# Kernel tuning notes

Measured on AMD Instinct MI355X. Metric: run time of the kernel, lower is better.

Reference implementation:

```python
import jax, jax.numpy as jnp
import numpy as np
from jax import lax

FEAT = 384        # features
FFN = 768         # ffn_features (chunk=True -> halves of 384)
ZDIM = FFN // 2   # 384
HID = 192         # AE hidden
B, N = 4, 128
LN_EPS = 1e-5


def gelu(x):
    return jax.nn.gelu(x, approximate=False)  # torch nn.GELU default = exact erf


def setup_inputs() -> dict:
    key = jax.random.key(0)
    ks = jax.random.split(key, 12)

    def lin(k, fan_in, shape):
        bound = 1.0 / np.sqrt(fan_in)
        return jax.random.uniform(k, shape, jnp.float32, -bound, bound)

    return {
        "x": jax.random.normal(ks[0], (B, N, FEAT), jnp.float32),
        "U_w": lin(ks[1], FEAT, (FEAT, FFN)),
        "U_b": lin(ks[2], FEAT, (FFN,)),
        "ln_w": jnp.ones((ZDIM,), jnp.float32),
        "ln_b": jnp.zeros((ZDIM,), jnp.float32),
        "enc_w": lin(ks[3], ZDIM, (ZDIM, HID)),
        "enc_b": lin(ks[4], ZDIM, (HID,)),
        "dec_w": lin(ks[5], HID, (HID, ZDIM)),
        "dec_b": lin(ks[6], HID, (ZDIM,)),
        "V_w": lin(ks[7], ZDIM, (ZDIM, FEAT)),
        "V_b": lin(ks[8], ZDIM, (FEAT,)),
    }


def _ae(z, enc_w, enc_b, dec_w, dec_b):
    h = gelu(z @ enc_w + enc_b)
    return h @ dec_w + dec_b


def reference(x, U_w, U_b, ln_w, ln_b, enc_w, enc_b, dec_w, dec_b, V_w, V_b):
    h = gelu(x @ U_w + U_b)                    # (B,N,FFN)
    xh, z = jnp.split(h, 2, axis=-1)           # chunk=True: (B,N,ZDIM) each
    z = lax.stop_gradient(z)                   # z.detach()
    mu = jnp.mean(z, axis=-1, keepdims=True)
    var = jnp.var(z, axis=-1, keepdims=True)
    z = (z - mu) / jnp.sqrt(var + LN_EPS) * ln_w + ln_b

    n = z.shape[1]
    eye = jnp.eye(n, dtype=z.dtype)
    # z_mask[b,i,j,:] = z[b,j,:] if i==j else 0   (mask_type='zeros')
    z_mask = eye[None, :, :, None] * z[:, None, :, :]   # (B,N,N,ZDIM)
    preds = _ae(z_mask, enc_w, enc_b, dec_w, dec_b)      # (B,N,N,ZDIM)
    dist = jnp.einsum('bijf,bjf->bij', preds, z)         # (B,N,N)
    attn = lax.stop_gradient(jax.nn.softmax(dist, axis=-1))
    out = jnp.einsum('bij,bjf->bif', attn, xh)           # (B,N,ZDIM)
    return out @ V_w + V_b                               # (B,N,FEAT)
```

## Files before the change

### kernel.cpp

```cpp
#include <hip/hip_runtime.h>
#include <hip/hip_bf16.h>
#include <math.h>

#define FEAT 384
#define FFN  768
#define ZDIM 384
#define HID  192
#define BB   4
#define NN   128
#define BN   (BB*NN)

__device__ __forceinline__ float gelu_exact(float x) {
    return 0.5f * x * (1.0f + erff(x * 0.70710678118654752440f));
}

__device__ __forceinline__ float bflo(unsigned u) { return __uint_as_float(u << 16); }
__device__ __forceinline__ float bfhi(unsigned u) { return __uint_as_float(u & 0xFFFF0000u); }

template<bool F32>
__device__ __forceinline__ float ldg(const void* p, int i) {
    if constexpr (F32) return ((const float*)p)[i];
    return __uint_as_float(((unsigned)((const unsigned short*)p)[i]) << 16);
}

__device__ __forceinline__ unsigned pack2(float a, float b) {
    __hip_bfloat16 ba = __float2bfloat16(a), bb = __float2bfloat16(b);
    unsigned short ua, ub;
    __builtin_memcpy(&ua, &ba, 2);
    __builtin_memcpy(&ub, &bb, 2);
    return (unsigned)ua | ((unsigned)ub << 16);
}

template<bool F32>
__device__ __forceinline__ void st8(void* p, size_t off, const float v[8]) {
    if constexpr (F32) {
        *(float4*)((float*)p + off)     = make_float4(v[0], v[1], v[2], v[3]);
        *(float4*)((float*)p + off + 4) = make_float4(v[4], v[5], v[6], v[7]);
    } else {
        uint4 u;
        u.x = pack2(v[0], v[1]); u.y = pack2(v[2], v[3]);
        u.z = pack2(v[4], v[5]); u.w = pack2(v[6], v[7]);
        *(uint4*)((unsigned short*)p + off) = u;
    }
}

template<bool F32> struct V8;
template<> struct V8<true> {
    float4 a, b;
    __device__ __forceinline__ void load(const void* p, size_t off) {
        a = *(const float4*)((const float*)p + off);
        b = *(const float4*)((const float*)p + off + 4);
    }
    __device__ __forceinline__ float g(int i) const {
        return (i < 4) ? (&a.x)[i] : (&b.x)[i - 4];
    }
};
template<> struct V8<false> {
    uint4 u;
    __device__ __forceinline__ void load(const void* p, size_t off) {
        u = *(const uint4*)((const unsigned short*)p + off);
    }
    __device__ __forceinline__ float g(int i) const {
        const unsigned w = (&u.x)[i >> 1];
        return (i & 1) ? bfhi(w) : bflo(w);
    }
};
template<bool F32> struct V4;
template<> struct V4<true> {
    float4 a;
    __device__ __forceinline__ void load(const void* p, size_t off) {
        a = *(const float4*)((const float*)p + off);
    }
    __device__ __forceinline__ float g(int i) const { return (&a.x)[i]; }
};
template<> struct V4<false> {
    uint2 u;
    __device__ __forceinline__ void load(const void* p, size_t off) {
        u = *(const uint2*)((const unsigned short*)p + off);
    }
    __device__ __forceinline__ float g(int i) const {
        const unsigned w = (&u.x)[i >> 1];
        return (i & 1) ? bfhi(w) : bflo(w);
    }
};

__device__ __forceinline__ bool is_f32(const void* ln_w) {
    return ((const unsigned short*)ln_w)[0] == 0;
}

__device__ __forceinline__ float block_sum(float v, float* sm) {
    for (int o = 32; o > 0; o >>= 1) v += __shfl_down(v, o, 64);
    const int lane = threadIdx.x & 63, w = threadIdx.x >> 6;
    __syncthreads();
    if (lane == 0) sm[w] = v;
    __syncthreads();
    return sm[0] + sm[1] + sm[2] + sm[3] + sm[4] + sm[5];
}
__device__ __forceinline__ float2 block_sum2(float vx, float vy, float* sm) {
    for (int o = 32; o > 0; o >>= 1) {
        vx += __shfl_down(vx, o, 64);
        vy += __shfl_down(vy, o, 64);
    }
    const int lane = threadIdx.x & 63, w = threadIdx.x >> 6;
    __syncthreads();
    if (lane == 0) { sm[w] = vx; sm[w + 6] = vy; }
    __syncthreads();
    return make_float2(sm[0] + sm[1] + sm[2] + sm[3] + sm[4] + sm[5],
                       sm[6] + sm[7] + sm[8] + sm[9] + sm[10] + sm[11]);
}
__device__ __forceinline__ float block_max(float v, float* sm) {
    for (int o = 32; o > 0; o >>= 1) v = fmaxf(v, __shfl_down(v, o, 64));
    const int lane = threadIdx.x & 63, w = threadIdx.x >> 6;
    __syncthreads();
    if (lane == 0) sm[w] = v;
    __syncthreads();
    return fmaxf(fmaxf(fmaxf(sm[0], sm[1]), fmaxf(sm[2], sm[3])), fmaxf(sm[4], sm[5]));
}

template<bool F32>
__device__ void rows_body(
    const void* __restrict__ x, const void* __restrict__ U_w,
    const void* __restrict__ U_b, const void* __restrict__ ln_w,
    const void* __restrict__ ln_b, const void* __restrict__ enc_w,
    const void* __restrict__ enc_b, const void* __restrict__ dec_w,
    const void* __restrict__ dec_b,
    float* __restrict__ xh, float* __restrict__ d0, float* __restrict__ diag)
{
    const int g = blockIdx.x;
    const int r0 = 2 * g, r1 = r0 + 1;
    const int t = threadIdx.x;
    __shared__ float xs[2][FEAT];
    __shared__ float zs[2][ZDIM];
    __shared__ float hid[2][HID];
    __shared__ float gh[HID];
    __shared__ float part[4608];
    __shared__ float sm[12];

    xs[0][t] = ldg<F32>(x, r0 * FEAT + t);
    xs[1][t] = ldg<F32>(x, r1 * FEAT + t);
    if (t < HID) gh[t] = gelu_exact(ldg<F32>(enc_b, t));
    __syncthreads();

    const int cgU = t % 96, khU = t / 96;
    const int cU = 8 * cgU;
    float acc0[8] = {0,0,0,0,0,0,0,0}, acc1[8] = {0,0,0,0,0,0,0,0};
    {
        const int kb = 96 * khU;
        V8<F32> wa[8], wb[8];
        #pragma unroll
        for (int j = 0; j < 8; j++) wa[j].load(U_w, (size_t)(kb + j) * FFN + cU);
        for (int k0 = kb; k0 < kb + 96; k0 += 16) {
            #pragma unroll
            for (int j = 0; j < 8; j++) wb[j].load(U_w, (size_t)(k0 + 8 + j) * FFN + cU);
            #pragma unroll
            for (int j = 0; j < 8; j++) {
                const float x0 = xs[0][k0 + j], x1 = xs[1][k0 + j];
                #pragma unroll
                for (int i = 0; i < 8; i++) {
                    const float w = wa[j].g(i);
                    acc0[i] = fmaf(x0, w, acc0[i]);
                    acc1[i] = fmaf(x1, w, acc1[i]);
                }
            }
            if (k0 + 16 < kb + 96) {
                #pragma unroll
                for (int j = 0; j < 8; j++) wa[j].load(U_w, (size_t)(k0 + 16 + j) * FFN + cU);
            }
            #pragma unroll
            for (int j = 0; j < 8; j++) {
                const float x0 = xs[0][k0 + 8 + j], x1 = xs[1][k0 + 8 + j];
                #pragma unroll
                for (int i = 0; i < 8; i++) {
                    const float w = wb[j].g(i);
                    acc0[i] = fmaf(x0, w, acc0[i]);
                    acc1[i] = fmaf(x1, w, acc1[i]);
                }
            }
        }
    }
    if (khU > 0) {
        float* p0 = &part[(size_t)(khU - 1) * 1536 + cU];
        #pragma unroll
        for (int i = 0; i < 8; i++) { p0[i] = acc0[i]; p0[768 + i] = acc1[i]; }
    }
    __syncthreads();

    float h0[8], h1[8];
    float s1a = 0.f, s1b = 0.f, s2a = 0.f, s2b = 0.f;
    if (khU == 0) {
        #pragma unroll
        for (int i = 0; i < 8; i++) {
            const int c = cU + i;
            const float ub = ldg<F32>(U_b, c);
            float v0 = acc0[i] + part[c] + part[1536 + c] + part[3072 + c] + ub;
            float v1 = acc1[i] + part[768 + c] + part[1536 + 768 + c] + part[3072 + 768 + c] + ub;
            v0 = gelu_exact(v0); v1 = gelu_exact(v1);
            h0[i] = v0; h1[i] = v1;
            if (cgU >= 48) { s1a += v0; s2a += v0 * v0; s1b += v1; s2b += v1 * v1; }
        }
        if (cgU < 48) {
            *(float4*)(xh + (size_t)r0 * ZDIM + cU)     = make_float4(h0[0], h0[1], h0[2], h0[3]);
            *(float4*)(xh + (size_t)r0 * ZDIM + cU + 4) = make_float4(h0[4], h0[5], h0[6], h0[7]);
            *(float4*)(xh + (size_t)r1 * ZDIM + cU)     = make_float4(h1[0], h1[1], h1[2], h1[3]);
            *(float4*)(xh + (size_t)r1 * ZDIM + cU + 4) = make_float4(h1[4], h1[5], h1[6], h1[7]);
        }
    }
    const float2 S1 = block_sum2(s1a, s1b, sm);
    const float2 S2 = block_sum2(s2a, s2b, sm);
    const float mu0 = S1.x * (1.0f / ZDIM), mu1 = S1.y * (1.0f / ZDIM);
    const float rs0 = rsqrtf(S2.x * (1.0f / ZDIM) - mu0 * mu0 + 1e-5f);
    const float rs1 = rsqrtf(S2.y * (1.0f / ZDIM) - mu1 * mu1 + 1e-5f);
    if (khU == 0 && cgU >= 48) {
        #pragma unroll
        for (int i = 0; i < 8; i++) {
            const int zc = cU - ZDIM + i;
            const float w = ldg<F32>(ln_w, zc), bb = ldg<F32>(ln_b, zc);
            zs[0][zc] = (h0[i] - mu0) * rs0 * w + bb;
            zs[1][zc] = (h1[i] - mu1) * rs1 * w + bb;
        }
    }
    __syncthreads();

    {
        const int cg = t % 48, kh = t / 48;
        const int cE = 4 * cg, kb = 48 * kh;
        float e0a[4] = {0,0,0,0}, e1a[4] = {0,0,0,0};
        V4<F32> ea[8], eb[8];
        #pragma unroll
        for (int j = 0; j < 8; j++) ea[j].load(enc_w, (size_t)(kb + j) * HID + cE);
        for (int k0 = kb; k0 < kb + 48; k0 += 16) {
            #pragma unroll
            for (int j = 0; j < 8; j++) eb[j].load(enc_w, (size_t)(k0 + 8 + j) * HID + cE);
            #pragma unroll
            for (int j = 0; j < 8; j++) {
                const float z0 = zs[0][k0 + j], z1 = zs[1][k0 + j];
                #pragma unroll
                for (int i = 0; i < 4; i++) {
                    const float w = ea[j].g(i);
                    e0a[i] = fmaf(z0, w, e0a[i]);
                    e1a[i] = fmaf(z1, w, e1a[i]);
                }
            }
            if (k0 + 16 < kb + 48) {
                #pragma unroll
                for (int j = 0; j < 8; j++) ea[j].load(enc_w, (size_t)(k0 + 16 + j) * HID + cE);
            }
            #pragma unroll
            for (int j = 0; j < 8; j++) {
                const float z0 = zs[0][k0 + 8 + j], z1 = zs[1][k0 + 8 + j];
                #pragma unroll
                for (int i = 0; i < 4; i++) {
                    const float w = eb[j].g(i);
                    e0a[i] = fmaf(z0, w, e0a[i]);
                    e1a[i] = fmaf(z1, w, e1a[i]);
                }
            }
        }
        if (kh > 0) {
            float* p = &part[(size_t)(kh - 1) * 384 + cE];
            #pragma unroll
            for (int i = 0; i < 4; i++) { p[i] = e0a[i]; p[192 + i] = e1a[i]; }
        }
        __syncthreads();
        if (kh == 0) {
            #pragma unroll
            for (int i = 0; i < 4; i++) {
                const int c = cE + i;
                float v0 = e0a[i], v1 = e1a[i];
                #pragma unroll
                for (int kk = 0; kk < 7; kk++) {
                    v0 += part[kk * 384 + c];
                    v1 += part[kk * 384 + 192 + c];
                }
                const float ebv = ldg<F32>(enc_b, c);
                hid[0][c] = gelu_exact(v0 + ebv);
                hid[1][c] = gelu_exact(v1 + ebv);
            }
        }
        __syncthreads();
    }

    {
        const int cg = t % 96, kh = t / 96;
        const int cD = 4 * cg, kb = 48 * kh;
        float a0[4] = {0,0,0,0}, a1[4] = {0,0,0,0}, a2[4] = {0,0,0,0};
        V4<F32> da[8], db_[8];
        #pragma unroll
        for (int j = 0; j < 8; j++) da[j].load(dec_w, (size_t)(kb + j) * ZDIM + cD);
        for (int k0 = kb; k0 < kb + 48; k0 += 16) {
            #pragma unroll
            for (int j = 0; j < 8; j++) db_[j].load(dec_w, (size_t)(k0 + 8 + j) * ZDIM + cD);
            #pragma unroll
            for (int j = 0; j < 8; j++) {
                const float v0 = hid[0][k0 + j], v1 = hid[1][k0 + j], gv = gh[k0 + j];
                #pragma unroll
                for (int i = 0; i < 4; i++) {
                    const float w = da[j].g(i);
                    a0[i] = fmaf(v0, w, a0[i]);
                    a1[i] = fmaf(v1, w, a1[i]);
                    a2[i] = fmaf(gv, w, a2[i]);
                }
            }
            if (k0 + 16 < kb + 48) {
                #pragma unroll
                for (int j = 0; j < 8; j++) da[j].load(dec_w, (size_t)(k0 + 16 + j) * ZDIM + cD);
            }
            #pragma unroll
            for (int j = 0; j < 8; j++) {
                const float v0 = hid[0][k0 + 8 + j], v1 = hid[1][k0 + 8 + j], gv = gh[k0 + 8 + j];
                #pragma unroll
                for (int i = 0; i < 4; i++) {
                    const float w = db_[j].g(i);
                    a0[i] = fmaf(v0, w, a0[i]);
                    a1[i] = fmaf(v1, w, a1[i]);
                    a2[i] = fmaf(gv, w, a2[i]);
                }
            }
        }
        if (kh > 0) {
            float* p = &part[(size_t)(kh - 1) * 1152 + cD];
            #pragma unroll
            for (int i = 0; i < 4; i++) { p[i] = a0[i]; p[384 + i] = a1[i]; p[768 + i] = a2[i]; }
        }
        __syncthreads();
        float pd0 = 0.f, pd1 = 0.f, pe0 = 0.f, pe1 = 0.f;
        if (kh == 0) {
            #pragma unroll
            for (int i = 0; i < 4; i++) {
                const int c = cD + i;
                const float dbv = ldg<F32>(dec_b, c);
                const float v0 = a0[i] + part[c] + part[1152 + c] + part[2304 + c] + dbv;
                const float v1 = a1[i] + part[384 + c] + part[1152 + 384 + c] + part[2304 + 384 + c] + dbv;
                const float v2 = a2[i] + part[768 + c] + part[1152 + 768 + c] + part[2304 + 768 + c] + dbv;
                const float z0 = zs[0][c], z1 = zs[1][c];
                pd0 = fmaf(v0, z0, pd0);
                pd1 = fmaf(v1, z1, pd1);
                pe0 = fmaf(v2, z0, pe0);
                pe1 = fmaf(v2, z1, pe1);
            }
        }
        const float2 DG = block_sum2(pd0, pd1, sm);
        const float2 DD = block_sum2(pe0, pe1, sm);
        if (t == 0) {
            diag[r0] = DG.x; diag[r1] = DG.y;
            d0[r0] = DD.x;   d0[r1] = DD.y;
        }
    }
}

__global__ __launch_bounds__(384) void k_rows(
    const void* x, const void* U_w, const void* U_b,
    const void* ln_w, const void* ln_b,
    const void* enc_w, const void* enc_b,
    const void* dec_w, const void* dec_b,
    float* xh, float* d0, float* diag)
{
    if (is_f32(ln_w))
        rows_body<true >(x, U_w, U_b, ln_w, ln_b, enc_w, enc_b, dec_w, dec_b, xh, d0, diag);
    else
        rows_body<false>(x, U_w, U_b, ln_w, ln_b, enc_w, enc_b, dec_w, dec_b, xh, d0, diag);
}

template<bool F32>
__device__ void out_body(
    const float* __restrict__ d0, const float* __restrict__ diag,
    const float* __restrict__ xh,
    const void* __restrict__ V_w, const void* __restrict__ V_b,
    void* __restrict__ out)
{
    const int g = blockIdx.x;
    const int r0 = 2 * g, r1 = r0 + 1;
    const int b = r0 >> 7;
    const int t = threadIdx.x;
    __shared__ float e0s[NN];
    __shared__ float as[2][ZDIM];
    __shared__ float pv[5376];
    __shared__ float sm[12];

    float d0v = -INFINITY, dgv = -INFINITY;
    if (t < NN) { d0v = d0[b * NN + t]; dgv = diag[b * NN + t]; }
    const float m = block_max(fmaxf(d0v, dgv), sm);
    float e0v = 0.f;
    if (t < NN) { e0v = expf(d0v - m); e0s[t] = e0v; }
    const float S = block_sum(e0v, sm);

    const float e00 = expf(d0[r0] - m), e01 = expf(d0[r1] - m);
    const float ed0 = expf(diag[r0] - m), ed1 = expf(diag[r1] - m);
    const float inv0 = 1.0f / (S - e00 + ed0);
    const float inv1 = 1.0f / (S - e01 + ed1);

    float acc = 0.f;
    {
        const float* xp = xh + (size_t)b * NN * ZDIM + t;
        float wa[16], wb[16];
        #pragma unroll
        for (int j = 0; j < 16; j++) wa[j] = xp[(size_t)j * ZDIM];
        for (int j0 = 0; j0 < NN; j0 += 32) {
            #pragma unroll
            for (int j = 0; j < 16; j++) wb[j] = xp[(size_t)(j0 + 16 + j) * ZDIM];
            #pragma unroll
            for (int j = 0; j < 16; j++) acc = fmaf(e0s[j0 + j], wa[j], acc);
            if (j0 + 32 < NN) {
                #pragma unroll
                for (int j = 0; j < 16; j++) wa[j] = xp[(size_t)(j0 + 32 + j) * ZDIM];
            }
            #pragma unroll
            for (int j = 0; j < 16; j++) acc = fmaf(e0s[j0 + 16 + j], wb[j], acc);
        }
    }
    as[0][t] = (acc + (ed0 - e00) * xh[(size_t)r0 * ZDIM + t]) * inv0;
    as[1][t] = (acc + (ed1 - e01) * xh[(size_t)r1 * ZDIM + t]) * inv1;
    __syncthreads();

    const int cg = t % 48, kh = t / 48;
    const int cV = 8 * cg, kb = 48 * kh;
    float a0[8] = {0,0,0,0,0,0,0,0}, a1[8] = {0,0,0,0,0,0,0,0};
    {
        V8<F32> va[8], vb[8];
        #pragma unroll
        for (int j = 0; j < 8; j++) va[j].load(V_w, (size_t)(kb + j) * FEAT + cV);
        for (int f0 = kb; f0 < kb + 48; f0 += 16) {
            #pragma unroll
            for (int j = 0; j < 8; j++) vb[j].load(V_w, (size_t)(f0 + 8 + j) * FEAT + cV);
            #pragma unroll
            for (int j = 0; j < 8; j++) {
                const float s0 = as[0][f0 + j], s1 = as[1][f0 + j];
                #pragma unroll
                for (int i = 0; i < 8; i++) {
                    const float w = va[j].g(i);
                    a0[i] = fmaf(s0, w, a0[i]);
                    a1[i] = fmaf(s1, w, a1[i]);
                }
            }
            if (f0 + 16 < kb + 48) {
                #pragma unroll
                for (int j = 0; j < 8; j++) va[j].load(V_w, (size_t)(f0 + 16 + j) * FEAT + cV);
            }
            #pragma unroll
            for (int j = 0; j < 8; j++) {
                const float s0 = as[0][f0 + 8 + j], s1 = as[1][f0 + 8 + j];
                #pragma unroll
                for (int i = 0; i < 8; i++) {
                    const float w = vb[j].g(i);
                    a0[i] = fmaf(s0, w, a0[i]);
                    a1[i] = fmaf(s1, w, a1[i]);
                }
            }
        }
    }
    if (kh > 0) {
        float* p = &pv[(size_t)(kh - 1) * 768 + cV];
        #pragma unroll
        for (int i = 0; i < 8; i++) { p[i] = a0[i]; p[384 + i] = a1[i]; }
    }
    __syncthreads();
    if (kh == 0) {
        float o0[8], o1[8];
        #pragma unroll
        for (int i = 0; i < 8; i++) {
            const int c = cV + i;
            const float vb_ = ldg<F32>(V_b, c);
            float u0 = a0[i] + vb_, u1 = a1[i] + vb_;
            #pragma unroll
            for (int kk = 0; kk < 7; kk++) {
                u0 += pv[kk * 768 + c];
                u1 += pv[kk * 768 + 384 + c];
            }
            o0[i] = u0; o1[i] = u1;
        }
        st8<F32>(out, (size_t)r0 * FEAT + cV, o0);
        st8<F32>(out, (size_t)r1 * FEAT + cV, o1);
    }
}

__global__ __launch_bounds__(384) void k_out(
    const void* ln_w,
    const float* d0, const float* diag, const float* xh,
    const void* V_w, const void* V_b, void* out)
{
    if (is_f32(ln_w))
        out_body<true >(d0, diag, xh, V_w, V_b, out);
    else
        out_body<false>(d0, diag, xh, V_w, V_b, out);
}

extern "C" void kernel_launch(void* const* d_in, const int* in_sizes, int n_in,
                              void* d_out, int out_size, void* d_ws, size_t ws_size,
                              hipStream_t stream) {
    const void* x     = d_in[0];
    const void* U_w   = d_in[1];
    const void* U_b   = d_in[2];
    const void* ln_w  = d_in[3];
    const void* ln_b  = d_in[4];
    const void* enc_w = d_in[5];
    const void* enc_b = d_in[6];
    const void* dec_w = d_in[7];
    const void* dec_b = d_in[8];
    const void* V_w   = d_in[9];
    const void* V_b   = d_in[10];

    float* ws   = (float*)d_ws;
    float* xh   = ws;
    float* d0   = xh + (size_t)BN * ZDIM;
    float* diag = d0 + BN;

    k_rows<<<BN / 2, 384, 0, stream>>>(x, U_w, U_b, ln_w, ln_b, enc_w, enc_b,
                                       dec_w, dec_b, xh, d0, diag);
    k_out<<<BN / 2, 384, 0, stream>>>(ln_w, d0, diag, xh, V_w, V_b, d_out);
}
```

Before: 111.7 us.

## Split per-row work across more blocks: one row per block, halves of FFN

Changes k_rows from two rows per block to one row per block, further split into two blocks that each compute one half of the U projection. The xh half writes its output and exits, and the z half runs LayerNorm, the autoencoder and the dot products. k_out likewise moves to one row per block. The aim is to raise parallelism from 256 blocks to 1024 and 512 so more CUs stay busy, at the cost of losing weight reuse across two rows and reading the weights more often.

Result: slower. 157.0 us (+40.5%).

```diff
diff --git a/kernel.cpp b/kernel.cpp
--- a/kernel.cpp
+++ b/kernel.cpp
@@ -126,225 +126,194 @@
     const void* __restrict__ dec_b,
     float* __restrict__ xh, float* __restrict__ d0, float* __restrict__ diag)
 {
-    const int g = blockIdx.x;
-    const int r0 = 2 * g, r1 = r0 + 1;
+    const int r = blockIdx.x >> 1;
+    const int h = blockIdx.x & 1;
     const int t = threadIdx.x;
-    __shared__ float xs[2][FEAT];
-    __shared__ float zs[2][ZDIM];
-    __shared__ float hid[2][HID];
+    __shared__ float xs[FEAT];
+    __shared__ float zs[ZDIM];
+    __shared__ float hid[HID];
     __shared__ float gh[HID];
-    __shared__ float part[4608];
+    __shared__ float part[7 * 384];
     __shared__ float sm[12];
 
-    xs[0][t] = ldg<F32>(x, r0 * FEAT + t);
-    xs[1][t] = ldg<F32>(x, r1 * FEAT + t);
-    if (t < HID) gh[t] = gelu_exact(ldg<F32>(enc_b, t));
-    __syncthreads();
-
-    const int cgU = t % 96, khU = t / 96;
-    const int cU = 8 * cgU;
-    float acc0[8] = {0,0,0,0,0,0,0,0}, acc1[8] = {0,0,0,0,0,0,0,0};
+    xs[t] = ldg<F32>(x, r * FEAT + t);
+    if (h && t < HID) gh[t] = gelu_exact(ldg<F32>(enc_b, t));
+    __syncthreads();
+
+    const int cg = t % 48, kh = t / 48;
+    const int cLoc = 8 * cg;
+    const int cGlob = 384 * h + cLoc;
+    const int kb = 48 * kh;
+    float acc[8] = {0,0,0,0,0,0,0,0};
     {
-        const int kb = 96 * khU;
         V8<F32> wa[8], wb[8];
         #pragma unroll
-        for (int j = 0; j < 8; j++) wa[j].load(U_w, (size_t)(kb + j) * FFN + cU);
-        for (int k0 = kb; k0 < kb + 96; k0 += 16) {
-            #pragma unroll
-            for (int j = 0; j < 8; j++) wb[j].load(U_w, (size_t)(k0 + 8 + j) * FFN + cU);
-            #pragma unroll
-            for (int j = 0; j < 8; j++) {
-                const float x0 = xs[0][k0 + j], x1 = xs[1][k0 + j];
-                #pragma unroll
-                for (int i = 0; i < 8; i++) {
-                    const float w = wa[j].g(i);
-                    acc0[i] = fmaf(x0, w, acc0[i]);
-                    acc1[i] = fmaf(x1, w, acc1[i]);
-                }
-            }
-            if (k0 + 16 < kb + 96) {
-                #pragma unroll
-                for (int j = 0; j < 8; j++) wa[j].load(U_w, (size_t)(k0 + 16 + j) * FFN + cU);
-            }
-            #pragma unroll
-            for (int j = 0; j < 8; j++) {
-                const float x0 = xs[0][k0 + 8 + j], x1 = xs[1][k0 + 8 + j];
-                #pragma unroll
-                for (int i = 0; i < 8; i++) {
-                    const float w = wb[j].g(i);
-                    acc0[i] = fmaf(x0, w, acc0[i]);
-                    acc1[i] = fmaf(x1, w, acc1[i]);
-                }
-            }
-        }
-    }
-    if (khU > 0) {
-        float* p0 = &part[(size_t)(khU - 1) * 1536 + cU];
-        #pragma unroll
-        for (int i = 0; i < 8; i++) { p0[i] = acc0[i]; p0[768 + i] = acc1[i]; }
-    }
-    __syncthreads();
-
-    float h0[8], h1[8];
-    float s1a = 0.f, s1b = 0.f, s2a = 0.f, s2b = 0.f;
-    if (khU == 0) {
+        for (int j = 0; j < 8; j++) wa[j].load(U_w, (size_t)(kb + j) * FFN + cGlob);
+        for (int k0 = kb; k0 < kb + 48; k0 += 16) {
+            #pragma unroll
+            for (int j = 0; j < 8; j++) wb[j].load(U_w, (size_t)(k0 + 8 + j) * FFN + cGlob);
+            #pragma unroll
+            for (int j = 0; j < 8; j++) {
+                const float xv = xs[k0 + j];
+                #pragma unroll
+                for (int i = 0; i < 8; i++) acc[i] = fmaf(xv, wa[j].g(i), acc[i]);
+            }
+            if (k0 + 16 < kb + 48) {
+                #pragma unroll
+                for (int j = 0; j < 8; j++) wa[j].load(U_w, (size_t)(k0 + 16 + j) * FFN + cGlob);
+            }
+            #pragma unroll
+            for (int j = 0; j < 8; j++) {
+                const float xv = xs[k0 + 8 + j];
+                #pragma unroll
+                for (int i = 0; i < 8; i++) acc[i] = fmaf(xv, wb[j].g(i), acc[i]);
+            }
+        }
+    }
+    if (kh > 0) {
+        float* p = &part[(kh - 1) * 384 + cLoc];
+        #pragma unroll
+        for (int i = 0; i < 8; i++) p[i] = acc[i];
+    }
+    __syncthreads();
+
+    float hv[8];
+    float s1 = 0.f, s2 = 0.f;
+    if (kh == 0) {
         #pragma unroll
         for (int i = 0; i < 8; i++) {
-            const int c = cU + i;
-            const float ub = ldg<F32>(U_b, c);
-            float v0 = acc0[i] + part[c] + part[1536 + c] + part[3072 + c] + ub;
-            float v1 = acc1[i] + part[768 + c] + part[1536 + 768 + c] + part[3072 + 768 + c] + ub;
-            v0 = gelu_exact(v0); v1 = gelu_exact(v1);
-            h0[i] = v0; h1[i] = v1;
-            if (cgU >= 48) { s1a += v0; s2a += v0 * v0; s1b += v1; s2b += v1 * v1; }
-        }
-        if (cgU < 48) {
-            *(float4*)(xh + (size_t)r0 * ZDIM + cU)     = make_float4(h0[0], h0[1], h0[2], h0[3]);
-            *(float4*)(xh + (size_t)r0 * ZDIM + cU + 4) = make_float4(h0[4], h0[5], h0[6], h0[7]);
-            *(float4*)(xh + (size_t)r1 * ZDIM + cU)     = make_float4(h1[0], h1[1], h1[2], h1[3]);
-            *(float4*)(xh + (size_t)r1 * ZDIM + cU + 4) = make_float4(h1[4], h1[5], h1[6], h1[7]);
-        }
-    }
-    const float2 S1 = block_sum2(s1a, s1b, sm);
-    const float2 S2 = block_sum2(s2a, s2b, sm);
-    const float mu0 = S1.x * (1.0f / ZDIM), mu1 = S1.y * (1.0f / ZDIM);
-    const float rs0 = rsqrtf(S2.x * (1.0f / ZDIM) - mu0 * mu0 + 1e-5f);
-    const float rs1 = rsqrtf(S2.y * (1.0f / ZDIM) - mu1 * mu1 + 1e-5f);
-    if (khU == 0 && cgU >= 48) {
+            float v = acc[i] + ldg<F32>(U_b, cGlob + i);
+            #pragma unroll
+            for (int kk = 0; kk < 7; kk++) v += part[kk * 384 + cLoc + i];
+            v = gelu_exact(v);
+            hv[i] = v;
+            s1 += v; s2 += v * v;
+        }
+        if (h == 0) {
+            *(float4*)(xh + (size_t)r * ZDIM + cLoc)     = make_float4(hv[0], hv[1], hv[2], hv[3]);
+            *(float4*)(xh + (size_t)r * ZDIM + cLoc + 4) = make_float4(hv[4], hv[5], hv[6], hv[7]);
+        }
+    }
+    if (h == 0) return;
+
+    const float2 S = block_sum2(s1, s2, sm);
+    const float mu = S.x * (1.0f / ZDIM);
+    const float rs = rsqrtf(S.y * (1.0f / ZDIM) - mu * mu + 1e-5f);
+    if (kh == 0) {
         #pragma unroll
         for (int i = 0; i < 8; i++) {
-            const int zc = cU - ZDIM + i;
-            const float w = ldg<F32>(ln_w, zc), bb = ldg<F32>(ln_b, zc);
-            zs[0][zc] = (h0[i] - mu0) * rs0 * w + bb;
-            zs[1][zc] = (h1[i] - mu1) * rs1 * w + bb;
+            const int zc = cLoc + i;
+            zs[zc] = (hv[i] - mu) * rs * ldg<F32>(ln_w, zc) + ldg<F32>(ln_b, zc);
         }
     }
     __syncthreads();
 
     {
-        const int cg = t % 48, kh = t / 48;
-        const int cE = 4 * cg, kb = 48 * kh;
-        float e0a[4] = {0,0,0,0}, e1a[4] = {0,0,0,0};
-        V4<F32> ea[8], eb[8];
-        #pragma unroll
-        for (int j = 0; j < 8; j++) ea[j].load(enc_w, (size_t)(kb + j) * HID + cE);
-        for (int k0 = kb; k0 < kb + 48; k0 += 16) {
-            #pragma unroll
-            for (int j = 0; j < 8; j++) eb[j].load(enc_w, (size_t)(k0 + 8 + j) * HID + cE);
-            #pragma unroll
-            for (int j = 0; j < 8; j++) {
-                const float z0 = zs[0][k0 + j], z1 = zs[1][k0 + j];
-                #pragma unroll
-                for (int i = 0; i < 4; i++) {
-                    const float w = ea[j].g(i);
-                    e0a[i] = fmaf(z0, w, e0a[i]);
-                    e1a[i] = fmaf(z1, w, e1a[i]);
-                }
-            }
-            if (k0 + 16 < kb + 48) {
-                #pragma unroll
-                for (int j = 0; j < 8; j++) ea[j].load(enc_w, (size_t)(k0 + 16 + j) * HID + cE);
-            }
-            #pragma unroll
-            for (int j = 0; j < 8; j++) {
-                const float z0 = zs[0][k0 + 8 + j], z1 = zs[1][k0 + 8 + j];
-                #pragma unroll
-                for (int i = 0; i < 4; i++) {
-                    const float w = eb[j].g(i);
-                    e0a[i] = fmaf(z0, w, e0a[i]);
-                    e1a[i] = fmaf(z1, w, e1a[i]);
-                }
-            }
-        }
-        if (kh > 0) {
-            float* p = &part[(size_t)(kh - 1) * 384 + cE];
-            #pragma unroll
-            for (int i = 0; i < 4; i++) { p[i] = e0a[i]; p[192 + i] = e1a[i]; }
+        const int cgE = t % 48, khE = t / 48;
+        const int cE = 4 * cgE, kbE = 48 * khE;
+        float ea[4] = {0,0,0,0};
+        V4<F32> va[8], vb[8];
+        #pragma unroll
+        for (int j = 0; j < 8; j++) va[j].load(enc_w, (size_t)(kbE + j) * HID + cE);
+        for (int k0 = kbE; k0 < kbE + 48; k0 += 16) {
+            #pragma unroll
+            for (int j = 0; j < 8; j++) vb[j].load(enc_w, (size_t)(k0 + 8 + j) * HID + cE);
+            #pragma unroll
+            for (int j = 0; j < 8; j++) {
+                const float zv = zs[k0 + j];
+                #pragma unroll
+                for (int i = 0; i < 4; i++) ea[i] = fmaf(zv, va[j].g(i), ea[i]);
+            }
+            if (k0 + 16 < kbE + 48) {
+                #pragma unroll
+                for (int j = 0; j < 8; j++) va[j].load(enc_w, (size_t)(k0 + 16 + j) * HID + cE);
+            }
+            #pragma unroll
+            for (int j = 0; j < 8; j++) {
+                const float zv = zs[k0 + 8 + j];
+                #pragma unroll
+                for (int i = 0; i < 4; i++) ea[i] = fmaf(zv, vb[j].g(i), ea[i]);
+            }
+        }
+        if (khE > 0) {
+            float* p = &part[(khE - 1) * 192 + cE];
+            #pragma unroll
+            for (int i = 0; i < 4; i++) p[i] = ea[i];
         }
         __syncthreads();
-        if (kh == 0) {
+        if (khE == 0) {
             #pragma unroll
             for (int i = 0; i < 4; i++) {
                 const int c = cE + i;
-                float v0 = e0a[i], v1 = e1a[i];
-                #pragma unroll
-                for (int kk = 0; kk < 7; kk++) {
-                    v0 += part[kk * 384 + c];
-                    v1 += part[kk * 384 + 192 + c];
+                float v = ea[i] + ldg<F32>(enc_b, c);
+                #pragma unroll
+                for (int kk = 0; kk < 7; kk++) v += part[kk * 192 + c];
+                hid[c] = gelu_exact(v);
+            }
+        }
+        __syncthreads();
+    }
+
+    {
+        const int cgD = t % 96, khD = t / 96;
+        const int cD = 4 * cgD, kbD = 48 * khD;
+        float aa[4] = {0,0,0,0}, ac[4] = {0,0,0,0};
+        V4<F32> va[8], vb[8];
+        #pragma unroll
+        for (int j = 0; j < 8; j++) va[j].load(dec_w, (size_t)(kbD + j) * ZDIM + cD);
+        for (int k0 = kbD; k0 < kbD + 48; k0 += 16) {
+            #pragma unroll
+            for (int j = 0; j < 8; j++) vb[j].load(dec_w, (size_t)(k0 + 8 + j) * ZDIM + cD);
+            #pragma unroll
+            for (int j = 0; j < 8; j++) {
+                const float hvv = hid[k0 + j], gv = gh[k0 + j];
+                #pragma unroll
+                for (int i = 0; i < 4; i++) {
+                    const float w = va[j].g(i);
+                    aa[i] = fmaf(hvv, w, aa[i]);
+                    ac[i] = fmaf(gv, w, ac[i]);
                 }
-                const float ebv = ldg<F32>(enc_b, c);
-                hid[0][c] = gelu_exact(v0 + ebv);
-                hid[1][c] = gelu_exact(v1 + ebv);
-            }
+            }
+            if (k0 + 16 < kbD + 48) {
+                #pragma unroll
+                for (int j = 0; j < 8; j++) va[j].load(dec_w, (size_t)(k0 + 16 + j) * ZDIM + cD);
+            }
+            #pragma unroll
+            for (int j = 0; j < 8; j++) {
+                const float hvv = hid[k0 + 8 + j], gv = gh[k0 + 8 + j];
+                #pragma unroll
+                for (int i = 0; i < 4; i++) {
+                    const float w = vb[j].g(i);
+                    aa[i] = fmaf(hvv, w, aa[i]);
+                    ac[i] = fmaf(gv, w, ac[i]);
+                }
+            }
+        }
+        if (khD > 0) {
+            float* p = &part[(khD - 1) * 768 + cD];
+            #pragma unroll
+            for (int i = 0; i < 4; i++) { p[i] = aa[i]; p[384 + i] = ac[i]; }
         }
         __syncthreads();
-    }
-
-    {
-        const int cg = t % 96, kh = t / 96;
-        const int cD = 4 * cg, kb = 48 * kh;
-        float a0[4] = {0,0,0,0}, a1[4] = {0,0,0,0}, a2[4] = {0,0,0,0};
-        V4<F32> da[8], db_[8];
-        #pragma unroll
-        for (int j = 0; j < 8; j++) da[j].load(dec_w, (size_t)(kb + j) * ZDIM + cD);
-        for (int k0 = kb; k0 < kb + 48; k0 += 16) {
-            #pragma unroll
-            for (int j = 0; j < 8; j++) db_[j].load(dec_w, (size_t)(k0 + 8 + j) * ZDIM + cD);
-            #pragma unroll
-            for (int j = 0; j < 8; j++) {
-                const float v0 = hid[0][k0 + j], v1 = hid[1][k0 + j], gv = gh[k0 + j];
-                #pragma unroll
-                for (int i = 0; i < 4; i++) {
-                    const float w = da[j].g(i);
-                    a0[i] = fmaf(v0, w, a0[i]);
-                    a1[i] = fmaf(v1, w, a1[i]);
-                    a2[i] = fmaf(gv, w, a2[i]);
-                }
-            }
-            if (k0 + 16 < kb + 48) {
-                #pragma unroll
-                for (int j = 0; j < 8; j++) da[j].load(dec_w, (size_t)(k0 + 16 + j) * ZDIM + cD);
-            }
-            #pragma unroll
-            for (int j = 0; j < 8; j++) {
-                const float v0 = hid[0][k0 + 8 + j], v1 = hid[1][k0 + 8 + j], gv = gh[k0 + 8 + j];
-                #pragma unroll
-                for (int i = 0; i < 4; i++) {
-                    const float w = db_[j].g(i);
-                    a0[i] = fmaf(v0, w, a0[i]);
-                    a1[i] = fmaf(v1, w, a1[i]);
-                    a2[i] = fmaf(gv, w, a2[i]);
-                }
-            }
-        }
-        if (kh > 0) {
-            float* p = &part[(size_t)(kh - 1) * 1152 + cD];
-            #pragma unroll
-            for (int i = 0; i < 4; i++) { p[i] = a0[i]; p[384 + i] = a1[i]; p[768 + i] = a2[i]; }
-        }
-        __syncthreads();
-        float pd0 = 0.f, pd1 = 0.f, pe0 = 0.f, pe1 = 0.f;
-        if (kh == 0) {
+        float pd = 0.f, pe = 0.f;
+        if (khD == 0) {
             #pragma unroll
             for (int i = 0; i < 4; i++) {
                 const int c = cD + i;
                 const float dbv = ldg<F32>(dec_b, c);
-                const float v0 = a0[i] + part[c] + part[1152 + c] + part[2304 + c] + dbv;
-                const float v1 = a1[i] + part[384 + c] + part[1152 + 384 + c] + part[2304 + 384 + c] + dbv;
-                const float v2 = a2[i] + part[768 + c] + part[1152 + 768 + c] + part[2304 + 768 + c] + dbv;
-                const float z0 = zs[0][c], z1 = zs[1][c];
-                pd0 = fmaf(v0, z0, pd0);
-                pd1 = fmaf(v1, z1, pd1);
-                pe0 = fmaf(v2, z0, pe0);
-                pe1 = fmaf(v2, z1, pe1);
-            }
-        }
-        const float2 DG = block_sum2(pd0, pd1, sm);
-        const float2 DD = block_sum2(pe0, pe1, sm);
-        if (t == 0) {
-            diag[r0] = DG.x; diag[r1] = DG.y;
-            d0[r0] = DD.x;   d0[r1] = DD.y;
-        }
+                float v = aa[i] + dbv, w = ac[i] + dbv;
+                #pragma unroll
+                for (int kk = 0; kk < 3; kk++) {
+                    v += part[kk * 768 + c];
+                    w += part[kk * 768 + 384 + c];
+                }
+                const float zv = zs[c];
+                pd = fmaf(v, zv, pd);
+                pe = fmaf(w, zv, pe);
+            }
+        }
+        const float2 D = block_sum2(pd, pe, sm);
+        if (t == 0) { diag[r] = D.x; d0[r] = D.y; }
     }
 }
 
@@ -368,13 +337,12 @@
     const void* __restrict__ V_w, const void* __restrict__ V_b,
     void* __restrict__ out)
 {
-    const int g = blockIdx.x;
-    const int r0 = 2 * g, r1 = r0 + 1;
-    const int b = r0 >> 7;
+    const int r = blockIdx.x;
+    const int b = r >> 7;
     const int t = threadIdx.x;
     __shared__ float e0s[NN];
-    __shared__ float as[2][ZDIM];
-    __shared__ float pv[5376];
+    __shared__ float as[ZDIM];
+    __shared__ float pv[7 * 384];
     __shared__ float sm[12];
 
     float d0v = -INFINITY, dgv = -INFINITY;
@@ -384,10 +352,9 @@
     if (t < NN) { e0v = expf(d0v - m); e0s[t] = e0v; }
     const float S = block_sum(e0v, sm);
 
-    const float e00 = expf(d0[r0] - m), e01 = expf(d0[r1] - m);
-    const float ed0 = expf(diag[r0] - m), ed1 = expf(diag[r1] - m);
-    const float inv0 = 1.0f / (S - e00 + ed0);
-    const float inv1 = 1.0f / (S - e01 + ed1);
+    const float e00 = expf(d0[r] - m);
+    const float ed0 = expf(diag[r] - m);
+    const float inv = 1.0f / (S - e00 + ed0);
 
     float acc = 0.f;
     {
@@ -408,13 +375,12 @@
             for (int j = 0; j < 16; j++) acc = fmaf(e0s[j0 + 16 + j], wb[j], acc);
         }
     }
-    as[0][t] = (acc + (ed0 - e00) * xh[(size_t)r0 * ZDIM + t]) * inv0;
-    as[1][t] = (acc + (ed1 - e01) * xh[(size_t)r1 * ZDIM + t]) * inv1;
+    as[t] = (acc + (ed0 - e00) * xh[(size_t)r * ZDIM + t]) * inv;
     __syncthreads();
 
     const int cg = t % 48, kh = t / 48;
     const int cV = 8 * cg, kb = 48 * kh;
-    float a0[8] = {0,0,0,0,0,0,0,0}, a1[8] = {0,0,0,0,0,0,0,0};
+    float a8[8] = {0,0,0,0,0,0,0,0};
     {
         V8<F32> va[8], vb[8];
         #pragma unroll
@@ -424,13 +390,9 @@
             for (int j = 0; j < 8; j++) vb[j].load(V_w, (size_t)(f0 + 8 + j) * FEAT + cV);
             #pragma unroll
             for (int j = 0; j < 8; j++) {
-                const float s0 = as[0][f0 + j], s1 = as[1][f0 + j];
-                #pragma unroll
-                for (int i = 0; i < 8; i++) {
-                    const float w = va[j].g(i);
-                    a0[i] = fmaf(s0, w, a0[i]);
-                    a1[i] = fmaf(s1, w, a1[i]);
-                }
+                const float s0 = as[f0 + j];
+                #pragma unroll
+                for (int i = 0; i < 8; i++) a8[i] = fmaf(s0, va[j].g(i), a8[i]);
             }
             if (f0 + 16 < kb + 48) {
                 #pragma unroll
@@ -438,38 +400,29 @@
             }
             #pragma unroll
             for (int j = 0; j < 8; j++) {
-                const float s0 = as[0][f0 + 8 + j], s1 = as[1][f0 + 8 + j];
-                #pragma unroll
-                for (int i = 0; i < 8; i++) {
-                    const float w = vb[j].g(i);
-                    a0[i] = fmaf(s0, w, a0[i]);
-                    a1[i] = fmaf(s1, w, a1[i]);
-                }
+                const float s0 = as[f0 + 8 + j];
+                #pragma unroll
+                for (int i = 0; i < 8; i++) a8[i] = fmaf(s0, vb[j].g(i), a8[i]);
             }
         }
     }
     if (kh > 0) {
-        float* p = &pv[(size_t)(kh - 1) * 768 + cV];
-        #pragma unroll
-        for (int i = 0; i < 8; i++) { p[i] = a0[i]; p[384 + i] = a1[i]; }
+        float* p = &pv[(kh - 1) * 384 + cV];
+        #pragma unroll
+        for (int i = 0; i < 8; i++) p[i] = a8[i];
     }
     __syncthreads();
     if (kh == 0) {
-        float o0[8], o1[8];
+        float o[8];
         #pragma unroll
         for (int i = 0; i < 8; i++) {
             const int c = cV + i;
-            const float vb_ = ldg<F32>(V_b, c);
-            float u0 = a0[i] + vb_, u1 = a1[i] + vb_;
-            #pragma unroll
-            for (int kk = 0; kk < 7; kk++) {
-                u0 += pv[kk * 768 + c];
-                u1 += pv[kk * 768 + 384 + c];
-            }
-            o0[i] = u0; o1[i] = u1;
-        }
-        st8<F32>(out, (size_t)r0 * FEAT + cV, o0);
-        st8<F32>(out, (size_t)r1 * FEAT + cV, o1);
+            float u = a8[i] + ldg<F32>(V_b, c);
+            #pragma unroll
+            for (int kk = 0; kk < 7; kk++) u += pv[kk * 384 + c];
+            o[i] = u;
+        }
+        st8<F32>(out, (size_t)r * FEAT + cV, o);
     }
 }
 
@@ -504,7 +457,7 @@
     float* d0   = xh + (size_t)BN * ZDIM;
     float* diag = d0 + BN;
 
-    k_rows<<<BN / 2, 384, 0, stream>>>(x, U_w, U_b, ln_w, ln_b, enc_w, enc_b,
+    k_rows<<<2 * BN, 384, 0, stream>>>(x, U_w, U_b, ln_w, ln_b, enc_w, enc_b,
                                        dec_w, dec_b, xh, d0, diag);
-    k_out<<<BN / 2, 384, 0, stream>>>(ln_w, d0, diag, xh, V_w, V_b, d_out);
-}
+    k_out<<<BN, 384, 0, stream>>>(ln_w, d0, diag, xh, V_w, V_b, d_out);
+}
```
